# Kernel optimization log

Hardware: AMD Instinct MI355X
Metric: run time of the kernel (lower is better)

The kernel has to match this reference:

```python
import jax, jax.numpy as jnp
import numpy as np

LAYER_DIM = 16
HALF = LAYER_DIM // 2  # 8
WIDTH = 8
SLOPE = 0.01  # nn.LeakyReLU default negative_slope


def _mlp(x, ws, bs):
    # 5 Linear layers with LeakyReLU between the first four; last is linear.
    for i in range(4):
        x = x @ ws[i].T + bs[i]
        x = jnp.where(x > 0, x, SLOPE * x)
    return x @ ws[4].T + bs[4]


def setup_inputs() -> dict:
    key = jax.random.key(0)
    ks = jax.random.split(key, 21)
    batch = 4_000_000
    z = jax.random.normal(ks[0], (batch, LAYER_DIM), dtype=jnp.float32)
    # layer dims: HALF -> 8 -> 8 -> 8 -> 8 -> HALF (all 8 when LAYER_DIM=16)
    dims = [HALF, WIDTH, WIDTH, WIDTH, WIDTH, HALF]
    ws_logs, bs_logs, ws_b, bs_b = [], [], [], []
    for i in range(5):
        fan_in, fan_out = dims[i], dims[i + 1]
        s = 1.0 / np.sqrt(fan_in)
        ws_logs.append(jax.random.uniform(ks[1 + i], (fan_out, fan_in), jnp.float32, -s, s))
        bs_logs.append(jax.random.uniform(ks[6 + i], (fan_out,), jnp.float32, -s, s))
        ws_b.append(jax.random.uniform(ks[11 + i], (fan_out, fan_in), jnp.float32, -s, s))
        bs_b.append(jax.random.uniform(ks[16 + i], (fan_out,), jnp.float32, -s, s))
    return {"z": z, "ws_logs": ws_logs, "bs_logs": bs_logs, "ws_b": ws_b, "bs_b": bs_b}


def reference(z, ws_logs, bs_logs, ws_b, bs_b):
    zl = z[:, :HALF]
    zr = z[:, HALF:]
    log_s = _mlp(zl, ws_logs, bs_logs)
    b = _mlp(zl, ws_b, bs_b)
    yr = jnp.exp(log_s) * zr + b
    return jnp.concatenate([zl, yr], axis=1)
```

## Files before the change

### kernel.cpp

```cpp
#include <hip/hip_runtime.h>

#define SLOPE 0.01f

typedef float f32x4 __attribute__((ext_vector_type(4)));

struct Half5 { const float* w[5]; const float* b[5]; };
struct WPtrs { Half5 logs; Half5 aff; };

__device__ __forceinline__ void mlp8(const Half5& h, const float x[8], float out[8]) {
    float a[8];
    #pragma unroll
    for (int j = 0; j < 8; ++j) a[j] = x[j];
    #pragma unroll
    for (int L = 0; L < 5; ++L) {
        const float* __restrict__ wl = h.w[L];
        const float* __restrict__ bl = h.b[L];
        float t[8];
        #pragma unroll
        for (int j = 0; j < 8; ++j) {
            float acc = bl[j];
            #pragma unroll
            for (int k = 0; k < 8; ++k)
                acc = fmaf(wl[j * 8 + k], a[k], acc);
            t[j] = acc;
        }
        #pragma unroll
        for (int j = 0; j < 8; ++j)
            a[j] = (L < 4) ? fmaxf(t[j], SLOPE * t[j]) : t[j];
    }
    #pragma unroll
    for (int j = 0; j < 8; ++j) out[j] = a[j];
}

#define ROWF4 5

__global__ void __launch_bounds__(256)
coupling_kernel(const f32x4* __restrict__ z,
                WPtrs p,
                f32x4* __restrict__ out,
                int batch) {
    __shared__ f32x4 lds[4][64 * ROWF4];

    const int tid  = threadIdx.x;
    const int lane = tid & 63;
    const int wv   = tid >> 6;
    f32x4* __restrict__ L = lds[wv];

    const long long waveRow0 = (long long)blockIdx.x * 256 + (long long)wv * 64;
    const long long f4base   = waveRow0 * 4;
    const long long f4limit  = (long long)batch * 4;
    const int a = lane >> 2;
    const int b = lane & 3;

    #pragma unroll
    for (int i = 0; i < 4; ++i) {
        long long gi = f4base + (long long)(i * 64 + lane);
        f32x4 t = {0.f, 0.f, 0.f, 0.f};
        if (gi < f4limit) t = z[gi];
        L[(i * 16 + a) * ROWF4 + b] = t;
    }

    const long long row = waveRow0 + lane;
    if (row < batch) {
        const int r0 = lane * ROWF4;
        f32x4 q0 = L[r0 + 0], q1 = L[r0 + 1];
        f32x4 q2 = L[r0 + 2], q3 = L[r0 + 3];

        float zl[8] = { q0.x, q0.y, q0.z, q0.w, q1.x, q1.y, q1.z, q1.w };
        float zr[8] = { q2.x, q2.y, q2.z, q2.w, q3.x, q3.y, q3.z, q3.w };

        float log_s[8], bb[8];
        mlp8(p.logs, zl, log_s);
        mlp8(p.aff,  zl, bb);

        float yr[8];
        #pragma unroll
        for (int k = 0; k < 8; ++k)
            yr[k] = fmaf(__expf(log_s[k]), zr[k], bb[k]);

        L[r0 + 2] = f32x4{ yr[0], yr[1], yr[2], yr[3] };
        L[r0 + 3] = f32x4{ yr[4], yr[5], yr[6], yr[7] };
    }

    #pragma unroll
    for (int i = 0; i < 4; ++i) {
        long long gi = f4base + (long long)(i * 64 + lane);
        if (gi < f4limit) {
            f32x4 o = L[(i * 16 + a) * ROWF4 + b];
            __builtin_nontemporal_store(o, out + gi);
        }
    }
}

extern "C" void kernel_launch(void* const* d_in, const int* in_sizes, int n_in,
                              void* d_out, int out_size, void* d_ws, size_t ws_size,
                              hipStream_t stream) {
    const int batch = in_sizes[0] / 16;

    WPtrs p;
    if (n_in >= 21) {
        for (int i = 0; i < 5; ++i) {
            p.logs.w[i] = (const float*)d_in[1 + i];
            p.logs.b[i] = (const float*)d_in[6 + i];
            p.aff.w[i]  = (const float*)d_in[11 + i];
            p.aff.b[i]  = (const float*)d_in[16 + i];
        }
    } else {
        const float* wl = (const float*)d_in[1];
        const float* bl = (const float*)d_in[2];
        const float* wv = (const float*)d_in[3];
        const float* bv = (const float*)d_in[4];
        for (int i = 0; i < 5; ++i) {
            p.logs.w[i] = wl + i * 64;
            p.logs.b[i] = bl + i * 8;
            p.aff.w[i]  = wv + i * 64;
            p.aff.b[i]  = bv + i * 8;
        }
    }

    int threads = 256;
    int blocks = (batch + threads - 1) / threads;
    coupling_kernel<<<blocks, threads, 0, stream>>>(
        (const f32x4*)d_in[0], p, (f32x4*)d_out, batch);
}
```

Baseline: 443.2 us.

## Use packed FMA for MLP layers and add full-block fast path with nontemporal loads

Rewrites the 8x8 dense layers so that pairs of outputs accumulate in two-wide float vectors with elementwise FMA and max, which lets the compiler emit packed FP32 instructions (v_pk_fma_f32) and roughly halves the ALU instruction count. Adds a per-block 'full' flag so that interior blocks skip bounds checks on load and store. Switches the input loads to nontemporal. Weight values are still read per element from pointers, so scalar loads and register pressure may limit the gain.

After: 410.5 us, median of 2. 7.4% less time.

```diff
diff --git a/kernel.cpp b/kernel.cpp
--- a/kernel.cpp
+++ b/kernel.cpp
@@ -3,6 +3,7 @@
 #define SLOPE 0.01f
 
 typedef float f32x4 __attribute__((ext_vector_type(4)));
+typedef float f32x2 __attribute__((ext_vector_type(2)));
 
 struct Half5 { const float* w[5]; const float* b[5]; };
 struct WPtrs { Half5 logs; Half5 aff; };
@@ -15,18 +16,27 @@
     for (int L = 0; L < 5; ++L) {
         const float* __restrict__ wl = h.w[L];
         const float* __restrict__ bl = h.b[L];
-        float t[8];
+        f32x2 t2[4];
         #pragma unroll
-        for (int j = 0; j < 8; ++j) {
-            float acc = bl[j];
+        for (int j2 = 0; j2 < 4; ++j2)
+            t2[j2] = f32x2{ bl[2 * j2], bl[2 * j2 + 1] };
+        #pragma unroll
+        for (int k = 0; k < 8; ++k) {
+            const f32x2 xa = { a[k], a[k] };
             #pragma unroll
-            for (int k = 0; k < 8; ++k)
-                acc = fmaf(wl[j * 8 + k], a[k], acc);
-            t[j] = acc;
+            for (int j2 = 0; j2 < 4; ++j2) {
+                const f32x2 w2 = { wl[(2 * j2) * 8 + k], wl[(2 * j2 + 1) * 8 + k] };
+                t2[j2] = __builtin_elementwise_fma(w2, xa, t2[j2]);
+            }
         }
         #pragma unroll
-        for (int j = 0; j < 8; ++j)
-            a[j] = (L < 4) ? fmaxf(t[j], SLOPE * t[j]) : t[j];
+        for (int j2 = 0; j2 < 4; ++j2) {
+            f32x2 v = t2[j2];
+            if (L < 4)
+                v = __builtin_elementwise_max(v, v * SLOPE);
+            a[2 * j2]     = v.x;
+            a[2 * j2 + 1] = v.y;
+        }
     }
     #pragma unroll
     for (int j = 0; j < 8; ++j) out[j] = a[j];
@@ -51,17 +61,25 @@
     const long long f4limit  = (long long)batch * 4;
     const int a = lane >> 2;
     const int b = lane & 3;
+    const bool full = ((long long)(blockIdx.x + 1) * 256) <= (long long)batch;
 
-    #pragma unroll
-    for (int i = 0; i < 4; ++i) {
-        long long gi = f4base + (long long)(i * 64 + lane);
-        f32x4 t = {0.f, 0.f, 0.f, 0.f};
-        if (gi < f4limit) t = z[gi];
-        L[(i * 16 + a) * ROWF4 + b] = t;
+    if (full) {
+        #pragma unroll
+        for (int i = 0; i < 4; ++i) {
+            f32x4 t = __builtin_nontemporal_load(z + f4base + (long long)(i * 64 + lane));
+            L[(i * 16 + a) * ROWF4 + b] = t;
+        }
+    } else {
+        #pragma unroll
+        for (int i = 0; i < 4; ++i) {
+            long long gi = f4base + (long long)(i * 64 + lane);
+            f32x4 t = {0.f, 0.f, 0.f, 0.f};
+            if (gi < f4limit) t = __builtin_nontemporal_load(z + gi);
+            L[(i * 16 + a) * ROWF4 + b] = t;
+        }
     }
 
-    const long long row = waveRow0 + lane;
-    if (row < batch) {
+    if (full || (waveRow0 + lane) < batch) {
         const int r0 = lane * ROWF4;
         f32x4 q0 = L[r0 + 0], q1 = L[r0 + 1];
         f32x4 q2 = L[r0 + 2], q3 = L[r0 + 3];
@@ -82,12 +100,20 @@
         L[r0 + 3] = f32x4{ yr[4], yr[5], yr[6], yr[7] };
     }
 
-    #pragma unroll
-    for (int i = 0; i < 4; ++i) {
-        long long gi = f4base + (long long)(i * 64 + lane);
-        if (gi < f4limit) {
+    if (full) {
+        #pragma unroll
+        for (int i = 0; i < 4; ++i) {
             f32x4 o = L[(i * 16 + a) * ROWF4 + b];
-            __builtin_nontemporal_store(o, out + gi);
+            __builtin_nontemporal_store(o, out + f4base + (long long)(i * 64 + lane));
+        }
+    } else {
+        #pragma unroll
+        for (int i = 0; i < 4; ++i) {
+            long long gi = f4base + (long long)(i * 64 + lane);
+            if (gi < f4limit) {
+                f32x4 o = L[(i * 16 + a) * ROWF4 + b];
+                __builtin_nontemporal_store(o, out + gi);
+            }
         }
     }
 }
```
